# Performance work log

Hardware: AMD Instinct MI355X
Metric: run time of the kernel (lower is better)

## Reference

```python
import jax, jax.numpy as jnp
import numpy as np

NUM_EMB = 60_000_000
EMB_DIM = 1
N_IDX = 4_000_000


def setup_inputs() -> dict:
    key = jax.random.key(0)
    k1, k2, k3 = jax.random.split(key, 3)
    emb = jnp.zeros((NUM_EMB, EMB_DIM), dtype=jnp.float32)
    x = jax.random.normal(k1, (N_IDX, EMB_DIM), dtype=jnp.float32)
    push_idx = jax.random.randint(k2, (N_IDX,), 0, NUM_EMB, dtype=jnp.int32)
    pull_idx = jax.random.randint(k3, (N_IDX,), 0, NUM_EMB, dtype=jnp.int32)
    return {"emb": emb, "x": x, "push_idx": push_idx, "pull_idx": pull_idx}


def reference(emb, x, push_idx, pull_idx):
    # push: emb[hash_idx] = x   (scatter-set into the [60M, 1] table)
    emb_new = emb.at[push_idx].set(x)
    # pull: x_emb = emb[hash_idx]  (gather)
    out = emb_new[pull_idx]  # [N_IDX, EMB_DIM]
    return out
```

## Files before the change

kernel.cpp:

```cpp
#include <hip/hip_runtime.h>
#include <stdint.h>


typedef unsigned long long u64;
typedef unsigned u32;

#define NB     512
#define BSHIFT 17
#define BLK    256
#define MBLK   1024
#define MB     4
#define VPT    16
#define CHUNK  (BLK * VPT)
#define CAP    12288
#define CPAD   16
#define TSLOTS 4096
#define TMASK  (TSLOTS - 1)
#define BBITS  131072
#define BWORDS (BBITS / 32)
#define BMASK  (BBITS - 1)

__device__ __forceinline__ u32 hkey(int key) { return (u32)key * 2654435761u; }

__global__ __launch_bounds__(BLK)
void scatter_kernel(const int* __restrict__ push_idx, int n_push, int gp,
                    const int* __restrict__ pull_idx, int n_pull,
                    int* __restrict__ cur_push, int* __restrict__ cur_pull,
                    u64* __restrict__ push_runs,
                    int* __restrict__ pull_keys, int* __restrict__ dest) {
    const bool is_push = (int)blockIdx.x < gp;
    const int* __restrict__ idx = is_push ? push_idx : pull_idx;
    const int n   = is_push ? n_push : n_pull;
    const int cid = is_push ? blockIdx.x : blockIdx.x - gp;
    int* __restrict__ cursors = is_push ? cur_push : cur_pull;

    __shared__ u64 buf[CHUNK];
    __shared__ int cnt[NB];
    __shared__ int basel[NB];
    __shared__ int baseg[NB];
    __shared__ int scan[NB];
    int t = threadIdx.x;
    for (int b = t; b < NB; b += BLK) cnt[b] = 0;
    __syncthreads();

    int base = cid * CHUNK;
    int   key_r[VPT];
    short bin_r[VPT];
    short pos_r[VPT];
    #pragma unroll
    for (int e = 0; e < VPT; ++e) {
        int i = base + e * BLK + t;
        if (i < n) {
            int key = idx[i];
            int b = key >> BSHIFT;
            key_r[e] = key;
            bin_r[e] = (short)b;
            pos_r[e] = (short)atomicAdd(&cnt[b], 1);
        } else bin_r[e] = -1;
    }
    __syncthreads();

    scan[t] = cnt[t]; scan[t + BLK] = cnt[t + BLK];
    __syncthreads();
    for (int d = 1; d < NB; d <<= 1) {
        int a0 = (t       >= d) ? scan[t       - d] : 0;
        int a1 = (t + BLK >= d) ? scan[t + BLK - d] : 0;
        __syncthreads();
        scan[t] += a0; scan[t + BLK] += a1;
        __syncthreads();
    }
    basel[t]       = scan[t]       - cnt[t];
    basel[t + BLK] = scan[t + BLK] - cnt[t + BLK];
    __syncthreads();

    for (int b = t; b < NB; b += BLK)
        if (cnt[b] > 0) baseg[b] = atomicAdd(&cursors[b * CPAD], cnt[b]);

    #pragma unroll
    for (int e = 0; e < VPT; ++e) {
        if (bin_r[e] >= 0) {
            int i = base + e * BLK + t;
            buf[basel[bin_r[e]] + pos_r[e]] =
                ((u64)(u32)key_r[e] << 32) | (u32)i;
        }
    }
    __syncthreads();

    int total = scan[NB - 1];
    for (int q = t; q < total; q += BLK) {
        u64 packed = buf[q];
        int key = (int)(packed >> 32);
        int b = key >> BSHIFT;
        int r = baseg[b] + (q - basel[b]);
        if (r < CAP) {
            int gpos = b * CAP + r;
            if (is_push) {
                push_runs[gpos] = packed;
            } else {
                pull_keys[gpos] = key;
                dest[(u32)packed] = gpos;
            }
        }
    }
}

__global__ __launch_bounds__(MBLK)
void match_kernel(const u64* __restrict__ push_runs,
                  const int* __restrict__ pull_keys,
                  const int* __restrict__ cur_push,
                  const int* __restrict__ cur_pull,
                  const float* __restrict__ x,
                  const float* __restrict__ emb,
                  float* __restrict__ staging) {
    __shared__ u32 bloom[BWORDS];
    __shared__ u64 tbl[TSLOTS];
    int b = blockIdx.x;
    int np = cur_push[b * CPAD]; np = np < CAP ? np : CAP;
    int nl = cur_pull[b * CPAD]; nl = nl < CAP ? nl : CAP;
    for (int i = threadIdx.x; i < BWORDS; i += MBLK) bloom[i] = 0u;
    for (int i = threadIdx.x; i < TSLOTS; i += MBLK) tbl[i] = 0ull;
    __syncthreads();

    const int* lkeys = pull_keys + (size_t)b * CAP;
    for (int i = threadIdx.x; i < nl; i += MBLK) {
        u32 h = hkey(lkeys[i]);
        atomicOr(&bloom[(h & BMASK) >> 5], 1u << (h & 31));
    }
    __syncthreads();

    const u64* prun = push_runs + (size_t)b * CAP;
    for (int i = threadIdx.x; i < np; i += MBLK) {
        u64 packed = prun[i];
        int key = (int)(packed >> 32);
        u32 h = hkey(key);
        if (!((bloom[(h & BMASK) >> 5] >> (h & 31)) & 1u)) continue;
        u32 key1 = (u32)key + 1u;
        u64 want = ((u64)key1 << 32) | ((u32)packed + 1u);
        u32 s = (h >> 20) & TMASK;
        for (;;) {
            u64 prev = atomicCAS(&tbl[s], 0ull, want);
            if (prev == 0ull) break;
            if ((prev >> 32) == key1) { atomicMax(&tbl[s], want); break; }
            s = (s + 1) & TMASK;
        }
    }
    __syncthreads();

    float* stg = staging + (size_t)b * CAP;
    const int STRIDE = MBLK * MB;
    for (int i = threadIdx.x * MB; i + MB <= nl; i += STRIDE) {
        int4 kk = *(const int4*)(lkeys + i);
        int k[MB] = {kk.x, kk.y, kk.z, kk.w};
        float g[MB];
        #pragma unroll
        for (int e = 0; e < MB; ++e) g[e] = emb[k[e]];
        u32 h[MB]; u64 tv[MB];
        #pragma unroll
        for (int e = 0; e < MB; ++e) h[e] = hkey(k[e]);
        #pragma unroll
        for (int e = 0; e < MB; ++e) tv[e] = tbl[(h[e] >> 20) & TMASK];
        float r[MB];
        #pragma unroll
        for (int e = 0; e < MB; ++e) {
            float v = g[e];
            u64 cur = tv[e];
            u32 key1 = (u32)k[e] + 1u;
            u32 s = (h[e] >> 20) & TMASK;
            while (cur != 0ull) {
                if ((cur >> 32) == key1) { v = x[(u32)cur - 1u]; break; }
                s = (s + 1) & TMASK;
                cur = tbl[s];
            }
            r[e] = v;
        }
        *(float4*)(stg + i) = make_float4(r[0], r[1], r[2], r[3]);
    }
    int tail = (nl / MB) * MB;
    for (int i = tail + threadIdx.x; i < nl; i += MBLK) {
        int key = lkeys[i];
        float v = emb[key];
        u32 h = hkey(key);
        u32 key1 = (u32)key + 1u;
        u32 s = (h >> 20) & TMASK;
        for (;;) {
            u64 cur = tbl[s];
            if (cur == 0ull) break;
            if ((cur >> 32) == key1) { v = x[(u32)cur - 1u]; break; }
            s = (s + 1) & TMASK;
        }
        stg[i] = v;
    }
}

__global__ __launch_bounds__(BLK)
void unpermute_kernel(const int* __restrict__ dest,
                      const float* __restrict__ staging,
                      float* __restrict__ out, int n) {
    int j0 = (blockIdx.x * BLK + threadIdx.x) * 4;
    if (j0 + 4 <= n) {
        int4 d = *(const int4*)(dest + j0);
        *(float4*)(out + j0) =
            make_float4(staging[d.x], staging[d.y], staging[d.z], staging[d.w]);
    } else {
        for (int j = j0; j < n; ++j) out[j] = staging[dest[j]];
    }
}

extern "C" void kernel_launch(void* const* d_in, const int* in_sizes, int n_in,
                              void* d_out, int out_size, void* d_ws, size_t ws_size,
                              hipStream_t stream) {
    const float* emb      = (const float*)d_in[0];
    const float* x        = (const float*)d_in[1];
    const int*   push_idx = (const int*)d_in[2];
    const int*   pull_idx = (const int*)d_in[3];
    float* out = (float*)d_out;

    const int n_push = in_sizes[2];
    const int n_pull = in_sizes[3];

    char* p = (char*)d_ws;
    int* cur_push = (int*)p;                  p += (size_t)NB * CPAD * 4;
    int* cur_pull = (int*)p;                  p += (size_t)NB * CPAD * 4;
    size_t zero_bytes = (size_t)(p - (char*)d_ws);
    u64*   push_runs = (u64*)p;               p += (size_t)NB * CAP * 8;
    int*   pull_keys = (int*)p;               p += (size_t)NB * CAP * 4;
    float* staging   = (float*)p;             p += (size_t)NB * CAP * 4;
    int*   dest      = (int*)p;               p += (size_t)n_pull * 4;

    hipMemsetAsync(d_ws, 0, zero_bytes, stream);

    int gp = (n_push + CHUNK - 1) / CHUNK;
    int gl = (n_pull + CHUNK - 1) / CHUNK;
    scatter_kernel<<<gp + gl, BLK, 0, stream>>>(
        push_idx, n_push, gp, pull_idx, n_pull,
        cur_push, cur_pull, push_runs, pull_keys, dest);
    match_kernel<<<NB, MBLK, 0, stream>>>(push_runs, pull_keys,
                                          cur_push, cur_pull, x, emb, staging);
    unpermute_kernel<<<(n_pull + BLK * 4 - 1) / (BLK * 4), BLK, 0, stream>>>(
        dest, staging, out, n_pull);
}
```

Baseline: 210.3 us.

## Replace random emb gather with windowed streaming through shared memory

Splits the match kernel in two. The first kernel streams each bin's contiguous 128K-float slice of the embedding table through shared memory in coalesced, double-buffered windows and fills staging from LDS. The second kernel handles only the push overrides, writing x values over matched staging entries. This swaps scattered 4-byte global gathers for sequential full-table reads. The cost is reading the whole table, scanning the pull keys once per window, and one extra kernel launch.

```diff
diff --git a/kernel.cpp b/kernel.cpp
--- a/kernel.cpp
+++ b/kernel.cpp
@@ -9,7 +9,6 @@
 #define BSHIFT 17
 #define BLK    256
 #define MBLK   1024
-#define MB     4
 #define VPT    16
 #define CHUNK  (BLK * VPT)
 #define CAP    12288
@@ -19,6 +18,8 @@
 #define BBITS  131072
 #define BWORDS (BBITS / 32)
 #define BMASK  (BBITS - 1)
+#define WFL    16384
+#define WCH    8
 
 __device__ __forceinline__ u32 hkey(int key) { return (u32)key * 2654435761u; }
 
@@ -105,18 +106,70 @@
 }
 
 __global__ __launch_bounds__(MBLK)
-void match_kernel(const u64* __restrict__ push_runs,
-                  const int* __restrict__ pull_keys,
-                  const int* __restrict__ cur_push,
-                  const int* __restrict__ cur_pull,
-                  const float* __restrict__ x,
-                  const float* __restrict__ emb,
-                  float* __restrict__ staging) {
+void window_gather_kernel(const int* __restrict__ pull_keys,
+                          const int* __restrict__ cur_pull,
+                          const float* __restrict__ emb, int num_emb,
+                          float* __restrict__ staging) {
+    __shared__ float win[WFL];
+    int b = blockIdx.x;
+    int nl = cur_pull[b * CPAD]; nl = nl < CAP ? nl : CAP;
+    if (nl == 0) return;
+    const int* lkeys = pull_keys + (size_t)b * CAP;
+    float* stg = staging + (size_t)b * CAP;
+    const int t = threadIdx.x;
+    const int nf4 = num_emb >> 2;
+    const int winbase4 = (b << BSHIFT) >> 2;
+    const float4* emb4 = (const float4*)emb;
+
+    float4 pf[4];
+    #pragma unroll
+    for (int k = 0; k < 4; ++k) {
+        int f4 = winbase4 + k * MBLK + t;
+        pf[k] = (f4 < nf4) ? emb4[f4] : make_float4(0.f, 0.f, 0.f, 0.f);
+    }
+    for (int c = 0; c < WCH; ++c) {
+        __syncthreads();
+        #pragma unroll
+        for (int k = 0; k < 4; ++k)
+            ((float4*)win)[k * MBLK + t] = pf[k];
+        __syncthreads();
+        if (c + 1 < WCH) {
+            #pragma unroll
+            for (int k = 0; k < 4; ++k) {
+                int f4 = winbase4 + (c + 1) * (WFL / 4) + k * MBLK + t;
+                pf[k] = (f4 < nf4) ? emb4[f4] : make_float4(0.f, 0.f, 0.f, 0.f);
+            }
+        }
+        int lo = (b << BSHIFT) + c * WFL;
+        for (int i = t * 4; i + 4 <= nl; i += MBLK * 4) {
+            int4 kk = *(const int4*)(lkeys + i);
+            int d0 = kk.x - lo, d1 = kk.y - lo, d2 = kk.z - lo, d3 = kk.w - lo;
+            if ((u32)d0 < (u32)WFL) stg[i]     = win[d0];
+            if ((u32)d1 < (u32)WFL) stg[i + 1] = win[d1];
+            if ((u32)d2 < (u32)WFL) stg[i + 2] = win[d2];
+            if ((u32)d3 < (u32)WFL) stg[i + 3] = win[d3];
+        }
+        int tail = nl & ~3;
+        for (int i = tail + t; i < nl; i += MBLK) {
+            int d = lkeys[i] - lo;
+            if ((u32)d < (u32)WFL) stg[i] = win[d];
+        }
+    }
+}
+
+__global__ __launch_bounds__(MBLK)
+void push_override_kernel(const u64* __restrict__ push_runs,
+                          const int* __restrict__ pull_keys,
+                          const int* __restrict__ cur_push,
+                          const int* __restrict__ cur_pull,
+                          const float* __restrict__ x,
+                          float* __restrict__ staging) {
     __shared__ u32 bloom[BWORDS];
     __shared__ u64 tbl[TSLOTS];
     int b = blockIdx.x;
     int np = cur_push[b * CPAD]; np = np < CAP ? np : CAP;
     int nl = cur_pull[b * CPAD]; nl = nl < CAP ? nl : CAP;
+    if (np == 0 || nl == 0) return;
     for (int i = threadIdx.x; i < BWORDS; i += MBLK) bloom[i] = 0u;
     for (int i = threadIdx.x; i < TSLOTS; i += MBLK) tbl[i] = 0ull;
     __syncthreads();
@@ -147,48 +200,38 @@
     __syncthreads();
 
     float* stg = staging + (size_t)b * CAP;
-    const int STRIDE = MBLK * MB;
-    for (int i = threadIdx.x * MB; i + MB <= nl; i += STRIDE) {
+    for (int i = threadIdx.x * 4; i + 4 <= nl; i += MBLK * 4) {
         int4 kk = *(const int4*)(lkeys + i);
-        int k[MB] = {kk.x, kk.y, kk.z, kk.w};
-        float g[MB];
-        #pragma unroll
-        for (int e = 0; e < MB; ++e) g[e] = emb[k[e]];
-        u32 h[MB]; u64 tv[MB];
-        #pragma unroll
-        for (int e = 0; e < MB; ++e) h[e] = hkey(k[e]);
-        #pragma unroll
-        for (int e = 0; e < MB; ++e) tv[e] = tbl[(h[e] >> 20) & TMASK];
-        float r[MB];
-        #pragma unroll
-        for (int e = 0; e < MB; ++e) {
-            float v = g[e];
+        int k[4] = {kk.x, kk.y, kk.z, kk.w};
+        u32 h[4]; u64 tv[4];
+        #pragma unroll
+        for (int e = 0; e < 4; ++e) h[e] = hkey(k[e]);
+        #pragma unroll
+        for (int e = 0; e < 4; ++e) tv[e] = tbl[(h[e] >> 20) & TMASK];
+        #pragma unroll
+        for (int e = 0; e < 4; ++e) {
             u64 cur = tv[e];
             u32 key1 = (u32)k[e] + 1u;
             u32 s = (h[e] >> 20) & TMASK;
             while (cur != 0ull) {
-                if ((cur >> 32) == key1) { v = x[(u32)cur - 1u]; break; }
+                if ((cur >> 32) == key1) { stg[i + e] = x[(u32)cur - 1u]; break; }
                 s = (s + 1) & TMASK;
                 cur = tbl[s];
             }
-            r[e] = v;
-        }
-        *(float4*)(stg + i) = make_float4(r[0], r[1], r[2], r[3]);
-    }
-    int tail = (nl / MB) * MB;
+        }
+    }
+    int tail = nl & ~3;
     for (int i = tail + threadIdx.x; i < nl; i += MBLK) {
         int key = lkeys[i];
-        float v = emb[key];
         u32 h = hkey(key);
         u32 key1 = (u32)key + 1u;
         u32 s = (h >> 20) & TMASK;
         for (;;) {
             u64 cur = tbl[s];
             if (cur == 0ull) break;
-            if ((cur >> 32) == key1) { v = x[(u32)cur - 1u]; break; }
+            if ((cur >> 32) == key1) { stg[i] = x[(u32)cur - 1u]; break; }
             s = (s + 1) & TMASK;
         }
-        stg[i] = v;
     }
 }
 
@@ -215,8 +258,9 @@
     const int*   pull_idx = (const int*)d_in[3];
     float* out = (float*)d_out;
 
-    const int n_push = in_sizes[2];
-    const int n_pull = in_sizes[3];
+    const int num_emb = in_sizes[0];
+    const int n_push  = in_sizes[2];
+    const int n_pull  = in_sizes[3];
 
     char* p = (char*)d_ws;
     int* cur_push = (int*)p;                  p += (size_t)NB * CPAD * 4;
@@ -234,8 +278,10 @@
     scatter_kernel<<<gp + gl, BLK, 0, stream>>>(
         push_idx, n_push, gp, pull_idx, n_pull,
         cur_push, cur_pull, push_runs, pull_keys, dest);
-    match_kernel<<<NB, MBLK, 0, stream>>>(push_runs, pull_keys,
-                                          cur_push, cur_pull, x, emb, staging);
+    window_gather_kernel<<<NB, MBLK, 0, stream>>>(pull_keys, cur_pull,
+                                                  emb, num_emb, staging);
+    push_override_kernel<<<NB, MBLK, 0, stream>>>(push_runs, pull_keys,
+                                                  cur_push, cur_pull, x, staging);
     unpermute_kernel<<<(n_pull + BLK * 4 - 1) / (BLK * 4), BLK, 0, stream>>>(
         dest, staging, out, n_pull);
 }
```

Measured after the change: 241.1 us. 1.15x slower.
